# Kernel tuning notes

Measured on AMD Instinct MI355X. Metric: run time of the kernel, lower is better.

The kernel has to match this reference:

```python
import jax, jax.numpy as jnp
import numpy as np

DIM = 1024
HEADS = 16
DIM_HEAD = 64
INNER = HEADS * DIM_HEAD  # 1024
SCALE = DIM_HEAD ** -0.5


def setup_inputs() -> dict:
    key = jax.random.key(0)
    k1, k2, k3, k4, k5 = jax.random.split(key, 5)
    x = jax.random.normal(k1, (4, 2048, DIM), dtype=jnp.float32)
    w_qkv = jax.random.normal(k2, (DIM, 3 * INNER), dtype=jnp.float32) * (DIM ** -0.5)
    b_qkv = jax.random.normal(k3, (3 * INNER,), dtype=jnp.float32) * 0.02
    w_out = jax.random.normal(k4, (INNER, DIM), dtype=jnp.float32) * (INNER ** -0.5)
    b_out = jax.random.normal(k5, (DIM,), dtype=jnp.float32) * 0.02
    return {"x": x, "w_qkv": w_qkv, "b_qkv": b_qkv, "w_out": w_out, "b_out": b_out}


def reference(x, w_qkv, b_qkv, w_out, b_out):
    b, n, _ = x.shape
    qkv = x @ w_qkv + b_qkv  # [b, n, 3*inner]
    q, k, v = jnp.split(qkv, 3, axis=-1)
    # b n (h d) -> b h n d
    def split_heads(t):
        return t.reshape(b, n, HEADS, DIM_HEAD).transpose(0, 2, 1, 3)
    q, k, v = map(split_heads, (q, k, v))
    scores = jnp.einsum('bhnd,bhmd->bhnm', q, k) * SCALE  # [b, h, n, n]
    att = jax.nn.softmax(scores, axis=-1)
    out = jnp.einsum('bhnm,bhmd->bhnd', att, v)  # [b, h, n, d]
    out = out.transpose(0, 2, 1, 3).reshape(b, n, INNER)  # b h n d -> b n (h d)
    return out @ w_out + b_out
```

## Files before the change

kernel.cpp:

```cpp
#include <hip/hip_runtime.h>
#include <stdint.h>

typedef float f32x4 __attribute__((ext_vector_type(4)));
typedef short s16x8 __attribute__((ext_vector_type(8)));
typedef unsigned short u16;
typedef unsigned short u16x4v __attribute__((ext_vector_type(4)));
typedef unsigned int u32x2 __attribute__((ext_vector_type(2)));

__device__ __forceinline__ u16 f2bf(float x) {
  union { float f; uint32_t u; } c; c.f = x;
  uint32_t u = c.u + 0x7fffu + ((c.u >> 16) & 1u);
  return (u16)(u >> 16);
}

__device__ __forceinline__ void async16(void* lds, const void* g) {
  __builtin_amdgcn_global_load_lds(
      (const __attribute__((address_space(1))) uint32_t*)(uintptr_t)g,
      (__attribute__((address_space(3))) uint32_t*)(uintptr_t)lds,
      16, 0, 0);
}

__device__ __forceinline__ uint32_t pack_bf2(float f0, float f1) {
  uint32_t u0 = __builtin_bit_cast(uint32_t, f0) + 0x8000u;
  uint32_t u1 = __builtin_bit_cast(uint32_t, f1) + 0x8000u;
  return __builtin_amdgcn_perm(u1, u0, 0x07060302u);
}

#define CSCALE 0.18033688011112042f

__global__ __launch_bounds__(256) void cvt_bf16_kernel(
    const float* __restrict__ in, u16* __restrict__ out) {
  size_t i = ((size_t)blockIdx.x * 256 + threadIdx.x) * 4;
  f32x4 v = *(const f32x4*)(in + i);
  u16x4v o;
#pragma unroll
  for (int j = 0; j < 4; ++j) o[j] = f2bf(v[j]);
  *(u16x4v*)(out + i) = o;
}

__global__ __launch_bounds__(256) void transpose_cvt(
    const float* __restrict__ in, u16* __restrict__ out, int R, int C) {
  __shared__ float t[32][33];
  int tx = threadIdx.x & 31, ty = threadIdx.x >> 5;
  int r0 = blockIdx.y * 32, c0 = blockIdx.x * 32;
#pragma unroll
  for (int i = 0; i < 4; ++i)
    t[ty + i * 8][tx] = in[(size_t)(r0 + ty + i * 8) * C + c0 + tx];
  __syncthreads();
#pragma unroll
  for (int i = 0; i < 4; ++i)
    out[(size_t)(c0 + ty + i * 8) * R + r0 + tx] = f2bf(t[tx][ty + i * 8]);
}

template <int MODE>
__global__ __launch_bounds__(512, 2) void gemm_bt(
    const u16* __restrict__ A, const u16* __restrict__ Bt,
    const float* __restrict__ bias,
    u16* __restrict__ qd, u16* __restrict__ kd, u16* __restrict__ vtd,
    float* __restrict__ outd) {
  __shared__ u16 lA[3][256 * 64];
  __shared__ u16 lB[3][128 * 64];
  const int tid = threadIdx.x;
  const int lane = tid & 63;
  const int quad = lane >> 4;
  const int l15 = lane & 15;
  const int wv = tid >> 6;
  const int wm = wv >> 1;
  const int wn = wv & 1;

  constexpr int GX = (MODE == 0) ? 24 : 8;
  const int bid = blockIdx.y * GX + blockIdx.x;
  const int xcd = bid & 7;
  const int jj = bid >> 3;
  const int m0 = (xcd * 4 + (jj & 3)) * 256;
  const int n0 = (jj >> 2) * 128;

  const char* aSrc0; const char* aSrc1; const char* aSrc2; const char* aSrc3;
  const char* bSrc0; const char* bSrc1;
  int aOff0, aOff1, aOff2, aOff3, bOff0, bOff1;
  {
    int c, r, s, g;
    c = 0 * 512 + tid; r = c >> 3; s = c & 7; g = s ^ (r & 7);
    aSrc0 = (const char*)A + (size_t)(m0 + r) * 2048 + g * 16; aOff0 = c * 16;
    c = 1 * 512 + tid; r = c >> 3; s = c & 7; g = s ^ (r & 7);
    aSrc1 = (const char*)A + (size_t)(m0 + r) * 2048 + g * 16; aOff1 = c * 16;
    c = 2 * 512 + tid; r = c >> 3; s = c & 7; g = s ^ (r & 7);
    aSrc2 = (const char*)A + (size_t)(m0 + r) * 2048 + g * 16; aOff2 = c * 16;
    c = 3 * 512 + tid; r = c >> 3; s = c & 7; g = s ^ (r & 7);
    aSrc3 = (const char*)A + (size_t)(m0 + r) * 2048 + g * 16; aOff3 = c * 16;
    c = 0 * 512 + tid; r = c >> 3; s = c & 7; g = s ^ (r & 7);
    bSrc0 = (const char*)Bt + (size_t)(n0 + r) * 2048 + g * 16; bOff0 = c * 16;
    c = 1 * 512 + tid; r = c >> 3; s = c & 7; g = s ^ (r & 7);
    bSrc1 = (const char*)Bt + (size_t)(n0 + r) * 2048 + g * 16; bOff1 = c * 16;
  }

  f32x4 acc[4][4] = {};
  const int swA = l15 & 7;
  const int aBase = (wm * 64 + l15) * 128;
  const int bBase = (wn * 64 + l15) * 128;
  const int swz0 = (quad ^ swA) * 16;
  const int swz1 = ((4 | quad) ^ swA) * 16;
  const char* lAc = (const char*)lA;
  const char* lBc = (const char*)lB;
  char* lAw = (char*)lA;
  char* lBw = (char*)lB;

#define GPH(CB, NB, KH, KO, STG)                                              \
  {                                                                           \
    s16x8 af[4], bq[4];                                                       \
    const int so = (KH) ? swz1 : swz0;                                        \
    _Pragma("unroll") for (int i = 0; i < 4; ++i)                             \
      af[i] = *(const s16x8*)(lAc + (CB) * 32768 + aBase + i * 2048 + so);    \
    _Pragma("unroll") for (int j = 0; j < 4; ++j)                             \
      bq[j] = *(const s16x8*)(lBc + (CB) * 16384 + bBase + j * 2048 + so);    \
    if (STG) {                                                                \
      if ((KH) == 0) {                                                        \
        async16(lAw + (NB) * 32768 + aOff0, aSrc0 + (KO));                    \
        async16(lAw + (NB) * 32768 + aOff1, aSrc1 + (KO));                    \
        async16(lBw + (NB) * 16384 + bOff0, bSrc0 + (KO));                    \
      } else {                                                                \
        async16(lAw + (NB) * 32768 + aOff2, aSrc2 + (KO));                    \
        async16(lAw + (NB) * 32768 + aOff3, aSrc3 + (KO));                    \
        async16(lBw + (NB) * 16384 + bOff1, bSrc1 + (KO));                    \
      }                                                                       \
    }                                                                         \
    __builtin_amdgcn_sched_barrier(0);                                        \
    __builtin_amdgcn_s_barrier();                                             \
    asm volatile("s_waitcnt lgkmcnt(0)" ::: "memory");                        \
    __builtin_amdgcn_sched_barrier(0);                                        \
    __builtin_amdgcn_s_setprio(1);                                            \
    _Pragma("unroll") for (int i = 0; i < 4; ++i)                             \
      _Pragma("unroll") for (int j = 0; j < 4; ++j)                           \
        acc[i][j] = __builtin_amdgcn_mfma_f32_16x16x32_bf16(af[i], bq[j],     \
                                                            acc[i][j], 0, 0, 0); \
    __builtin_amdgcn_s_setprio(0);                                            \
    __builtin_amdgcn_sched_barrier(0);                                        \
  }

  async16(lAw + aOff0, aSrc0);
  async16(lAw + aOff1, aSrc1);
  async16(lAw + aOff2, aSrc2);
  async16(lAw + aOff3, aSrc3);
  async16(lBw + bOff0, bSrc0);
  async16(lBw + bOff1, bSrc1);
  async16(lAw + 32768 + aOff0, aSrc0 + 128);
  async16(lAw + 32768 + aOff1, aSrc1 + 128);
  async16(lAw + 32768 + aOff2, aSrc2 + 128);
  async16(lAw + 32768 + aOff3, aSrc3 + 128);
  async16(lBw + 16384 + bOff0, bSrc0 + 128);
  async16(lBw + 16384 + bOff1, bSrc1 + 128);
  asm volatile("s_waitcnt vmcnt(6)" ::: "memory");
  __builtin_amdgcn_s_barrier();

#define GTILE(T)                                                              \
  GPH((T) % 3, ((T) + 2) % 3, 0, ((T) + 2) * 128, 1);                         \
  GPH((T) % 3, ((T) + 2) % 3, 1, ((T) + 2) * 128, 1);                         \
  asm volatile("s_waitcnt vmcnt(6)" ::: "memory");                            \
  __builtin_amdgcn_s_barrier();

  GTILE(0) GTILE(1) GTILE(2) GTILE(3) GTILE(4) GTILE(5) GTILE(6)
  GTILE(7) GTILE(8) GTILE(9) GTILE(10) GTILE(11) GTILE(12) GTILE(13)
#undef GTILE

  GPH(2, 0, 0, 0, 0);
  GPH(2, 0, 1, 0, 0);
  asm volatile("s_waitcnt vmcnt(0)" ::: "memory");
  __builtin_amdgcn_s_barrier();
  GPH(0, 0, 0, 0, 0);
  GPH(0, 0, 1, 0, 0);
#undef GPH

  float bj[4];
#pragma unroll
  for (int j = 0; j < 4; ++j) bj[j] = bias[n0 + wn * 64 + j * 16 + l15];

  if (MODE == 0) {
#pragma unroll
    for (int j = 0; j < 4; ++j) {
      int col = n0 + wn * 64 + j * 16 + l15;
      int which = col >> 10;
      int rem = col & 1023;
      int h = rem >> 6, d = rem & 63;
#pragma unroll
      for (int i = 0; i < 4; ++i) {
#pragma unroll
        for (int r = 0; r < 4; ++r) {
          int row = m0 + wm * 64 + i * 16 + quad * 4 + r;
          int b = row >> 11, s = row & 2047;
          float t = acc[i][j][r] + bj[j];
          if (which == 0) t *= CSCALE;
          u16 v = f2bf(t);
          size_t bh = (size_t)(b * 16 + h);
          if (which == 0)      qd[(bh * 2048 + s) * 64 + d] = v;
          else if (which == 1) kd[(bh * 2048 + s) * 64 + d] = v;
          else                 vtd[(bh * 64 + d) * 2048 + s] = v;
        }
      }
    }
  } else {
#pragma unroll
    for (int i = 0; i < 4; ++i)
#pragma unroll
      for (int r = 0; r < 4; ++r) {
        int row = m0 + wm * 64 + i * 16 + quad * 4 + r;
#pragma unroll
        for (int j = 0; j < 4; ++j) {
          int col = n0 + wn * 64 + j * 16 + l15;
          outd[(size_t)row * 1024 + col] = acc[i][j][r] + bj[j];
        }
      }
  }
}

__global__ __launch_bounds__(256, 2) void attn_fused(
    const u16* __restrict__ Q, const u16* __restrict__ Kd,
    const u16* __restrict__ Vt, u16* __restrict__ Od) {
  __shared__ u16 lK[2][4096];
  __shared__ u16 lV[2][4096];
  const int tid = threadIdx.x;
  const int lane = tid & 63;
  const int wv = tid >> 6;
  const int quad = lane >> 4;
  const int l15 = lane & 15;
  const int bh = blockIdx.x & 63;
  const int qt = blockIdx.x >> 6;
  const int q0 = qt * 256 + wv * 64;

  const u16* qb = Q + ((size_t)bh * 2048 + q0) * 64;
  const char* kbB = (const char*)(Kd + (size_t)bh * 2048 * 64);
  const char* vbB = (const char*)(Vt + (size_t)bh * 64 * 2048);

  const int r0 = tid >> 3, s0 = tid & 7;
  const int r1 = r0 + 32;
  const int kOff0 = r0 * 128 + ((s0 ^ (r0 & 7)) * 16);
  const int kOff1 = r1 * 128 + ((s0 ^ (r1 & 7)) * 16);
  const int vOff0 = r0 * 4096 + ((s0 ^ (r0 & 7)) * 16);
  const int vOff1 = r1 * 4096 + ((s0 ^ (r1 & 7)) * 16);

  auto stage = [&](int kbase, int buf) {
    const char* ks = kbB + (size_t)kbase * 128;
    const char* vs = vbB + (size_t)kbase * 2;
    async16((char*)lK[buf] + tid * 16, ks + kOff0);
    async16((char*)lK[buf] + 4096 + tid * 16, ks + kOff1);
    async16((char*)lV[buf] + tid * 16, vs + vOff0);
    async16((char*)lV[buf] + 4096 + tid * 16, vs + vOff1);
  };

  s16x8 qfr[4][2];
#pragma unroll
  for (int qf = 0; qf < 4; ++qf)
#pragma unroll
    for (int kd2 = 0; kd2 < 2; ++kd2)
      qfr[qf][kd2] = *(const s16x8*)(qb + (qf * 16 + l15) * 64 + kd2 * 32 + quad * 8);

  s16x8 ones;
#pragma unroll
  for (int j = 0; j < 8; ++j) ones[j] = (short)0x3F80;

  f32x4 oacc[4][4] = {};
  f32x4 lacc[4] = {};

  const int sw = (l15 & 7);

  auto compute = [&](int buf) {
    const char* bK = (const char*)lK[buf];
    const char* bV = (const char*)lV[buf];

    uint32_t pd[4][4][2];
#pragma unroll
    for (int mf = 0; mf < 4; ++mf) {
      const char* kr = bK + (mf * 16 + l15) * 128;
      s16x8 kf0 = *(const s16x8*)(kr + ((quad ^ sw) * 16));
      s16x8 kf1 = *(const s16x8*)(kr + (((4 + quad) ^ sw) * 16));
      f32x4 st[4];
#pragma unroll
      for (int qf = 0; qf < 4; ++qf) {
        f32x4 a = {};
        a = __builtin_amdgcn_mfma_f32_16x16x32_bf16(kf0, qfr[qf][0], a, 0, 0, 0);
        a = __builtin_amdgcn_mfma_f32_16x16x32_bf16(kf1, qfr[qf][1], a, 0, 0, 0);
        st[qf] = a;
      }
#pragma unroll
      for (int qf = 0; qf < 4; ++qf) {
        float p0 = __builtin_amdgcn_exp2f(st[qf][0]);
        float p1 = __builtin_amdgcn_exp2f(st[qf][1]);
        float p2 = __builtin_amdgcn_exp2f(st[qf][2]);
        float p3 = __builtin_amdgcn_exp2f(st[qf][3]);
        pd[mf][qf][0] = pack_bf2(p0, p1);
        pd[mf][qf][1] = pack_bf2(p2, p3);
      }
    }

    s16x8 vf[4][2];
#pragma unroll
    for (int df = 0; df < 4; ++df) {
      const char* vr = bV + (df * 16 + l15) * 128;
#pragma unroll
      for (int kh = 0; kh < 2; ++kh)
        vf[df][kh] = *(const s16x8*)(vr + (((kh * 4 + quad) ^ sw) * 16));
    }

#pragma unroll
    for (int kh = 0; kh < 2; ++kh)
#pragma unroll
      for (int qf = 0; qf < 4; ++qf)
#pragma unroll
        for (int pi = 0; pi < 2; ++pi) {
          uint32_t x = pd[2 * kh][qf][pi];
          uint32_t y = pd[2 * kh + 1][qf][pi];
          asm("s_nop 1\n\t"
              "v_permlane32_swap_b32 %0, %1\n\t"
              "s_nop 0\n\t"
              "v_permlane16_swap_b32 %0, %1"
              : "+v"(x), "+v"(y));
          pd[2 * kh][qf][pi] = x;
          pd[2 * kh + 1][qf][pi] = y;
        }

#pragma unroll
    for (int kh = 0; kh < 2; ++kh)
#pragma unroll
      for (int qf = 0; qf < 4; ++qf) {
        union { s16x8 h; uint32_t u[4]; } bfr;
        bfr.u[0] = pd[2 * kh][qf][0];
        bfr.u[1] = pd[2 * kh][qf][1];
        bfr.u[2] = pd[2 * kh + 1][qf][0];
        bfr.u[3] = pd[2 * kh + 1][qf][1];
#pragma unroll
        for (int df = 0; df < 4; ++df)
          oacc[df][qf] = __builtin_amdgcn_mfma_f32_16x16x32_bf16(vf[df][kh], bfr.h, oacc[df][qf], 0, 0, 0);
        lacc[qf] = __builtin_amdgcn_mfma_f32_16x16x32_bf16(ones, bfr.h, lacc[qf], 0, 0, 0);
      }
  };

  stage(0, 0);
  __syncthreads();
#pragma unroll 1
  for (int t = 0; t < 32; t += 2) {
    if (t + 1 < 32) stage((t + 1) * 64, 1);
    compute(0);
    __syncthreads();
    if (t + 2 < 32) stage((t + 2) * 64, 0);
    compute(1);
    __syncthreads();
  }

  const int b = bh >> 4, h = bh & 15;
  float inv[4];
#pragma unroll
  for (int qf = 0; qf < 4; ++qf) inv[qf] = 1.0f / lacc[qf][0];
#pragma unroll
  for (int qf = 0; qf < 4; ++qf) {
    u16* rowp = Od + ((size_t)b * 2048 + q0 + qf * 16 + l15) * 1024 + h * 64;
#pragma unroll
    for (int df = 0; df < 4; ++df) {
      u32x2 w;
      w.x = pack_bf2(oacc[df][qf][0] * inv[qf], oacc[df][qf][1] * inv[qf]);
      w.y = pack_bf2(oacc[df][qf][2] * inv[qf], oacc[df][qf][3] * inv[qf]);
      *(u32x2*)(rowp + df * 16 + quad * 4) = w;
    }
  }
}

extern "C" void kernel_launch(void* const* d_in, const int* in_sizes, int n_in,
                              void* d_out, int out_size, void* d_ws, size_t ws_size,
                              hipStream_t stream) {
  const float* x = (const float*)d_in[0];
  const float* w_qkv = (const float*)d_in[1];
  const float* b_qkv = (const float*)d_in[2];
  const float* w_out = (const float*)d_in[3];
  const float* b_out = (const float*)d_in[4];
  float* out = (float*)d_out;
  char* ws = (char*)d_ws;

  u16* xb    = (u16*)(ws + 0);
  u16* wqkvT = (u16*)(ws + 16777216);
  u16* woutT = (u16*)(ws + 23068672);
  u16* qw    = (u16*)(ws + 25165824);
  u16* kw    = (u16*)(ws + 41943040);
  u16* vtw   = (u16*)(ws + 58720256);
  u16* attO  = (u16*)(ws + 75497472);

  cvt_bf16_kernel<<<8192, 256, 0, stream>>>(x, xb);
  transpose_cvt<<<dim3(96, 32), 256, 0, stream>>>(w_qkv, wqkvT, 1024, 3072);
  transpose_cvt<<<dim3(32, 32), 256, 0, stream>>>(w_out, woutT, 1024, 1024);
  gemm_bt<0><<<dim3(24, 32), 512, 0, stream>>>(xb, wqkvT, b_qkv, qw, kw, vtw, nullptr);
  attn_fused<<<512, 256, 0, stream>>>(qw, kw, vtw, attO);
  gemm_bt<1><<<dim3(8, 32), 512, 0, stream>>>(attO, woutT, b_out, nullptr, nullptr, nullptr, out);
}
```

Before: 252.8 us.

## Merge GEMM K half-phases into one tile step, dropping inner barriers and priority hints

Each K tile of the bf16 GEMM main loop used to run as two half-phases, each with its own LDS reads, partial async staging, a workgroup barrier, an lgkmcnt wait and s_setprio-wrapped MFMAs. The tile is now one step that reads both halves' fragments, issues all six async loads together, and interleaves the MFMAs, leaving only the barrier between tiles. The aim is to halve the barrier and wait overhead and let the compiler schedule LDS reads against MFMAs. It doubles the fragment registers held live, which could lower occupancy. It also drops the explicit sched_barrier and lgkmcnt(0) wait, so ordering now rests on compiler-inserted waits.

```diff
diff --git a/kernel.cpp b/kernel.cpp
--- a/kernel.cpp
+++ b/kernel.cpp
@@ -105,36 +105,32 @@
   char* lAw = (char*)lA;
   char* lBw = (char*)lB;
 
-#define GPH(CB, NB, KH, KO, STG)                                              \
+#define GTILE(CB, NB, KO, STG)                                                \
   {                                                                           \
-    s16x8 af[4], bq[4];                                                       \
-    const int so = (KH) ? swz1 : swz0;                                        \
+    s16x8 af0[4], bq0[4], af1[4], bq1[4];                                     \
+    _Pragma("unroll") for (int i = 0; i < 4; ++i) {                           \
+      af0[i] = *(const s16x8*)(lAc + (CB) * 32768 + aBase + i * 2048 + swz0); \
+      af1[i] = *(const s16x8*)(lAc + (CB) * 32768 + aBase + i * 2048 + swz1); \
+    }                                                                         \
+    _Pragma("unroll") for (int j = 0; j < 4; ++j) {                           \
+      bq0[j] = *(const s16x8*)(lBc + (CB) * 16384 + bBase + j * 2048 + swz0); \
+      bq1[j] = *(const s16x8*)(lBc + (CB) * 16384 + bBase + j * 2048 + swz1); \
+    }                                                                         \
+    if (STG) {                                                                \
+      async16(lAw + (NB) * 32768 + aOff0, aSrc0 + (KO));                      \
+      async16(lAw + (NB) * 32768 + aOff1, aSrc1 + (KO));                      \
+      async16(lAw + (NB) * 32768 + aOff2, aSrc2 + (KO));                      \
+      async16(lAw + (NB) * 32768 + aOff3, aSrc3 + (KO));                      \
+      async16(lBw + (NB) * 16384 + bOff0, bSrc0 + (KO));                      \
+      async16(lBw + (NB) * 16384 + bOff1, bSrc1 + (KO));                      \
+    }                                                                         \
     _Pragma("unroll") for (int i = 0; i < 4; ++i)                             \
-      af[i] = *(const s16x8*)(lAc + (CB) * 32768 + aBase + i * 2048 + so);    \
-    _Pragma("unroll") for (int j = 0; j < 4; ++j)                             \
-      bq[j] = *(const s16x8*)(lBc + (CB) * 16384 + bBase + j * 2048 + so);    \
-    if (STG) {                                                                \
-      if ((KH) == 0) {                                                        \
-        async16(lAw + (NB) * 32768 + aOff0, aSrc0 + (KO));                    \
-        async16(lAw + (NB) * 32768 + aOff1, aSrc1 + (KO));                    \
-        async16(lBw + (NB) * 16384 + bOff0, bSrc0 + (KO));                    \
-      } else {                                                                \
-        async16(lAw + (NB) * 32768 + aOff2, aSrc2 + (KO));                    \
-        async16(lAw + (NB) * 32768 + aOff3, aSrc3 + (KO));                    \
-        async16(lBw + (NB) * 16384 + bOff1, bSrc1 + (KO));                    \
+      _Pragma("unroll") for (int j = 0; j < 4; ++j) {                         \
+        acc[i][j] = __builtin_amdgcn_mfma_f32_16x16x32_bf16(af0[i], bq0[j],   \
+                                                            acc[i][j], 0, 0, 0); \
+        acc[i][j] = __builtin_amdgcn_mfma_f32_16x16x32_bf16(af1[i], bq1[j],   \
+                                                            acc[i][j], 0, 0, 0); \
       }                                                                       \
-    }                                                                         \
-    __builtin_amdgcn_sched_barrier(0);                                        \
-    __builtin_amdgcn_s_barrier();                                             \
-    asm volatile("s_waitcnt lgkmcnt(0)" ::: "memory");                        \
-    __builtin_amdgcn_sched_barrier(0);                                        \
-    __builtin_amdgcn_s_setprio(1);                                            \
-    _Pragma("unroll") for (int i = 0; i < 4; ++i)                             \
-      _Pragma("unroll") for (int j = 0; j < 4; ++j)                           \
-        acc[i][j] = __builtin_amdgcn_mfma_f32_16x16x32_bf16(af[i], bq[j],     \
-                                                            acc[i][j], 0, 0, 0); \
-    __builtin_amdgcn_s_setprio(0);                                            \
-    __builtin_amdgcn_sched_barrier(0);                                        \
   }
 
   async16(lAw + aOff0, aSrc0);
@@ -152,23 +148,20 @@
   asm volatile("s_waitcnt vmcnt(6)" ::: "memory");
   __builtin_amdgcn_s_barrier();
 
-#define GTILE(T)                                                              \
-  GPH((T) % 3, ((T) + 2) % 3, 0, ((T) + 2) * 128, 1);                         \
-  GPH((T) % 3, ((T) + 2) % 3, 1, ((T) + 2) * 128, 1);                         \
+#define GSTEP(T)                                                              \
+  GTILE((T) % 3, ((T) + 2) % 3, ((T) + 2) * 128, 1);                          \
   asm volatile("s_waitcnt vmcnt(6)" ::: "memory");                            \
   __builtin_amdgcn_s_barrier();
 
-  GTILE(0) GTILE(1) GTILE(2) GTILE(3) GTILE(4) GTILE(5) GTILE(6)
-  GTILE(7) GTILE(8) GTILE(9) GTILE(10) GTILE(11) GTILE(12) GTILE(13)
-#undef GTILE
-
-  GPH(2, 0, 0, 0, 0);
-  GPH(2, 0, 1, 0, 0);
+  GSTEP(0) GSTEP(1) GSTEP(2) GSTEP(3) GSTEP(4) GSTEP(5) GSTEP(6)
+  GSTEP(7) GSTEP(8) GSTEP(9) GSTEP(10) GSTEP(11) GSTEP(12) GSTEP(13)
+#undef GSTEP
+
+  GTILE(2, 0, 0, 0);
   asm volatile("s_waitcnt vmcnt(0)" ::: "memory");
   __builtin_amdgcn_s_barrier();
-  GPH(0, 0, 0, 0, 0);
-  GPH(0, 0, 1, 0, 0);
-#undef GPH
+  GTILE(0, 0, 0, 0);
+#undef GTILE
 
   float bj[4];
 #pragma unroll
```

After: 275.4 us. 8.9% more time.
